# Optimization experiments

Measured on AMD Instinct MI355X. Metric: run time of the kernel, lower is better.

Reference implementation:

```python
import jax, jax.numpy as jnp
from jax import lax
import numpy as np

B, T = 256, 100
N_FEAT, V, E, H = 64, 32, 8, 512
CAT_POS = np.arange(0, N_FEAT, 4)                                 # 16 categorical feature indices
CONT_POS = np.array([k for k in range(N_FEAT) if k % 4 != 0])      # 48 continuous feature indices
N_CAT, N_CONT = len(CAT_POS), len(CONT_POS)
IN_LEN = N_FEAT + N_CAT * (E - 1)                                  # 176, matches input_linear.in_features
N_LAYERS = 2                                                        # len(hidden_layers) - 1 LSTMs

# Precompute the interleaved output layout of embed(): walking feature index k,
# categorical features occupy E slots, continuous features 1 slot.
def _layout():
    cont_off, cat_off, cur = [], [], 0
    for k in range(N_FEAT):
        if k % 4 == 0:
            cat_off.append(cur); cur += E
        else:
            cont_off.append(cur); cur += 1
    return np.array(cont_off), np.array(cat_off)
CONT_OFF, CAT_OFF = _layout()
CAT_COLS = (CAT_OFF[:, None] + np.arange(E)).ravel()               # [N_CAT*E] target columns


def lstm(x, Wih, Whh, bih, bhh):
    # PyTorch LSTM, batch_first, gate order (i, f, g, o).
    xw = jnp.einsum('bti,gi->btg', x, Wih) + bih                   # [B,T,4H] input projection (one GEMM)
    def step(carry, xw_t):
        h, c = carry
        gates = xw_t + h @ Whh.T + bhh
        i, f, g, o = jnp.split(gates, 4, axis=-1)
        c = jax.nn.sigmoid(f) * c + jax.nn.sigmoid(i) * jnp.tanh(g)
        h = jax.nn.sigmoid(o) * jnp.tanh(c)
        return (h, c), h
    h0 = jnp.zeros((x.shape[0], Whh.shape[1]), x.dtype)
    (_, _), hs = lax.scan(step, (h0, h0), jnp.swapaxes(xw, 0, 1))
    return jnp.swapaxes(hs, 0, 1)                                   # [B,T,H]


def setup_inputs() -> dict:
    key = jax.random.key(0)
    ks = jax.random.split(key, 16)
    s = 0.05
    base = jax.random.normal(ks[0], (B, T, N_FEAT), jnp.float32)
    cats = jax.random.randint(ks[1], (B, T, N_CAT), 0, V)
    x = base.at[..., CAT_POS].set(cats.astype(jnp.float32))
    return {
        'x': x,
        'scaler_mean': jax.random.normal(ks[2], (N_FEAT,), jnp.float32),
        'scaler_scale': jax.random.uniform(ks[3], (N_FEAT,), jnp.float32, minval=0.5, maxval=2.0),
        'emb': jax.random.normal(ks[4], (N_CAT, V, E), jnp.float32) * s,
        'W_in': jax.random.normal(ks[5], (IN_LEN, H), jnp.float32) * s,
        'b_in': jnp.zeros((H,), jnp.float32),
        'Wih': jax.random.normal(ks[6], (N_LAYERS, 4 * H, H), jnp.float32) * s,
        'Whh': jax.random.normal(ks[7], (N_LAYERS, 4 * H, H), jnp.float32) * s,
        'bih': jnp.zeros((N_LAYERS, 4 * H), jnp.float32),
        'bhh': jnp.zeros((N_LAYERS, 4 * H), jnp.float32),
        'W_out': jax.random.normal(ks[8], (H, N_CONT), jnp.float32) * s,
        'b_out': jnp.zeros((N_CONT,), jnp.float32),
        'W_cls': jax.random.normal(ks[9], (N_CAT, H, V), jnp.float32) * s,
        'b_cls': jnp.zeros((N_CAT, V), jnp.float32),
    }


def reference(x, scaler_mean, scaler_scale, emb, W_in, b_in, Wih, Whh, bih, bhh, W_out, b_out, W_cls, b_cls):
    # ---- embed(): vectorized replacement of the triple python loop ----
    scaled = (x - scaler_mean) / scaler_scale                      # sklearn StandardScaler.transform
    cont_vals = scaled[..., CONT_POS]                              # [B,T,48]
    idx = x[..., CAT_POS].astype(jnp.int32)                        # [B,T,16] categorical codes
    embv = emb[jnp.arange(N_CAT)[None, None, :], idx]              # [B,T,16,E] gather
    new = jnp.zeros((x.shape[0], x.shape[1], IN_LEN), x.dtype)
    new = new.at[..., CONT_OFF].set(cont_vals)
    new = new.at[..., CAT_COLS].set(embv.reshape(x.shape[0], x.shape[1], N_CAT * E))
    # ---- input linear + activation ----
    h = jax.nn.relu(new @ W_in + b_in)                             # [B,T,512]
    # ---- stacked LSTMs, activation after each ----
    for l in range(N_LAYERS):
        h = jax.nn.relu(lstm(h, Wih[l], Whh[l], bih[l], bhh[l]))
    last = h[:, -1, :]                                             # [B,512]
    cont_out = last @ W_out + b_out                                # [B,48]
    cls_out = jnp.einsum('bh,nhv->bnv', last, W_cls) + b_cls       # [B,16,32] classification heads
    return (cont_out, cls_out)
```

## Files before the change

kernel.cpp:

```cpp
#include <hip/hip_runtime.h>

#define BB 256
#define TT 100
#define HH 512
#define G4 2048
#define INL 176
#define KIN 192
#define NCAT 16
#define NCONT 48
#define VV 32
#define EE 8
#define MTOT (BB*TT)
#define GRPB 32
#define FS 16
#define NW (2*2*G4*HH)

typedef unsigned short u16;
typedef unsigned int   u32;
typedef unsigned long long u64;
typedef __attribute__((ext_vector_type(8))) short bf16x8;
typedef __attribute__((ext_vector_type(4))) float f32x4;

__device__ __forceinline__ float bf2f(u16 u){
    union { u32 i; float f; } v; v.i = ((u32)u) << 16; return v.f;
}
__device__ __forceinline__ u16 f2bf(float f){
    union { float f; u32 i; } v; v.f = f;
    u32 b = v.i;
    b += 0x7FFFu + ((b >> 16) & 1u);
    return (u16)(b >> 16);
}
__device__ __forceinline__ float fast_tanh(float x){
    float e = __expf(2.f * x);
    return 1.f - 2.f / (e + 1.f);
}
__device__ __forceinline__ u64 relu4_bf16(u64 v){
    u64 s = v & 0x8000800080008000ULL;
    u64 m = s - (s >> 15);
    return v & ~(s | m);
}

__global__ void PredictionModel_58841051955204_kernel(
    const float* __restrict__ Win, u16* __restrict__ WinT,
    const float* __restrict__ Wih, u16* __restrict__ Wihb,
    const float* __restrict__ Whh, u16* __restrict__ Whhb){
    int idx = blockIdx.x*256 + threadIdx.x;
    if (idx < HH*KIN){
        int h = idx / KIN, i = idx % KIN;
        WinT[idx] = (i < INL) ? f2bf(Win[i*HH + h]) : (u16)0;
        return;
    }
    int c1 = idx - HH*KIN;
    if (c1 < 2*G4*HH){ Wihb[c1] = f2bf(Wih[c1]); return; }
    int c2 = c1 - 2*G4*HH;
    if (c2 < 2*G4*HH) Whhb[c2] = f2bf(Whh[c2]);
}

__global__ void k_feat(const float* __restrict__ x, const float* __restrict__ mean,
                       const float* __restrict__ scale, const float* __restrict__ emb,
                       u16* __restrict__ feat, int* __restrict__ bar){
    if (blockIdx.x == 0){
        for (int i = threadIdx.x; i < 4096; i += 256)
            __hip_atomic_store(&bar[i], 0, __ATOMIC_RELAXED, __HIP_MEMORY_SCOPE_AGENT);
    }
    int idx = blockIdx.x*256 + threadIdx.x;
    int bt = idx >> 4, g = idx & 15;
    if (bt >= MTOT) return;
    const float* xr = x + (size_t)bt*64;
    u16* fr = feat + (size_t)bt*KIN;
    int k0 = g*4;
    int ci = (int)xr[k0];
    if (ci < 0) ci = 0;
    if (ci > VV-1) ci = VV-1;
    const float* ep = emb + (size_t)(g*VV + ci)*EE;
    int c0 = g*11;
    for (int e = 0; e < 8; e++) fr[c0+e] = f2bf(ep[e]);
    for (int j = 1; j <= 3; j++){
        int k = k0 + j;
        fr[c0 + 8 + (j-1)] = f2bf((xr[k] - mean[k]) / scale[k]);
    }
    fr[INL + g] = 0;
}

__global__ __launch_bounds__(256) void k_gemm(
    const u16* __restrict__ A, int lda,
    const u16* __restrict__ W, int K,
    const float* __restrict__ bias1, const float* __restrict__ bias2,
    void* __restrict__ out, int ldo, int kc_cnt, int do_relu, int out_half)
{
    __shared__ u16 sA[64*40];
    __shared__ u16 sB[256*40];
    int tid = threadIdx.x;
    int w = tid >> 6, lane = tid & 63, q = lane >> 4, r = lane & 15;
    int m0 = blockIdx.x * 64;
    int n0 = blockIdx.y * 256;

    f32x4 acc[4][4];
    for (int a_ = 0; a_ < 4; a_++)
        for (int b_ = 0; b_ < 4; b_++){
            acc[a_][b_][0] = 0.f; acc[a_][b_][1] = 0.f;
            acc[a_][b_][2] = 0.f; acc[a_][b_][3] = 0.f;
        }

    for (int kc = 0; kc < kc_cnt; kc++){
        {
            int row = tid >> 2, seg = tid & 3;
            uint4 v = *(const uint4*)(A + (size_t)(m0+row)*lda + kc*32 + seg*8);
            *(uint4*)(&sA[row*40 + seg*8]) = v;
            const u16* wr = W + (size_t)(n0 + tid)*K + kc*32;
            uint4 b0 = *(const uint4*)(wr);
            uint4 b1 = *(const uint4*)(wr+8);
            uint4 b2 = *(const uint4*)(wr+16);
            uint4 b3 = *(const uint4*)(wr+24);
            u16* d = &sB[tid*40];
            *(uint4*)(d)    = b0; *(uint4*)(d+8)  = b1;
            *(uint4*)(d+16) = b2; *(uint4*)(d+24) = b3;
        }
        __syncthreads();
        bf16x8 a[4], b[4];
        for (int mt = 0; mt < 4; mt++) a[mt] = *(const bf16x8*)(&sA[(mt*16 + r)*40 + q*8]);
        for (int i = 0; i < 4; i++)    b[i]  = *(const bf16x8*)(&sB[((w*4+i)*16 + r)*40 + q*8]);
        for (int mt = 0; mt < 4; mt++)
            for (int i = 0; i < 4; i++)
                acc[mt][i] = __builtin_amdgcn_mfma_f32_16x16x32_bf16(a[mt], b[i], acc[mt][i], 0, 0, 0);
        __syncthreads();
    }

    for (int i = 0; i < 4; i++){
        int n = n0 + (w*4+i)*16 + r;
        float bs = 0.f;
        if (bias1) bs += bias1[n];
        if (bias2) bs += bias2[n];
        for (int mt = 0; mt < 4; mt++){
            for (int reg = 0; reg < 4; reg++){
                int m = m0 + mt*16 + q*4 + reg;
                float v = acc[mt][i][reg] + bs;
                if (do_relu) v = fmaxf(v, 0.f);
                if (out_half) ((_Float16*)out)[(size_t)m*ldo + n] = (_Float16)v;
                else          ((u16*)out)[(size_t)m*ldo + n] = f2bf(v);
            }
        }
    }
}

__global__ __launch_bounds__(256, 1) void k_rec2(
    const u16* __restrict__ Wihb,
    const u16* __restrict__ Whhb,
    const u16* __restrict__ Xbuf,
    const float* __restrict__ bih, const float* __restrict__ bhh,
    u64* __restrict__ h0r,
    u64* __restrict__ h1A, u64* __restrict__ h1B,
    int* __restrict__ bar)
{
    extern __shared__ u16 smem[];
    int tid = threadIdx.x;
    int w = tid >> 6, lane = tid & 63, q = lane >> 4, r = lane & 15;
    int lay  = blockIdx.x >> 7;
    int bid7 = blockIdx.x & 127;
    int mg = bid7 & 3, jb = bid7 >> 2;
    int m0 = mg*64, j0 = jb*16;
    int j = j0 + r;
    int* F0x = bar;
    int* F1x = bar + 2048;
    int fidx = (mg*GRPB + jb)*FS;
    const u16* sWih = smem;
    const u16* sWhh = smem + 64*512;

    {
        int row = tid >> 2, seg = tid & 3;
        int g = row >> 4, jj = row & 15;
        const u16* srcI = Wihb + (size_t)lay*G4*HH + (size_t)(g*HH + j0 + jj)*HH;
        const u16* srcW = Whhb + (size_t)lay*G4*HH + (size_t)(g*HH + j0 + jj)*HH;
        for (int i = 0; i < 16; i++){
            int c = seg*16 + i;
            *(uint4*)(&smem[row*512 + ((c ^ (row & 7)) * 8)]) = *(const uint4*)(srcI + c*8);
            *(uint4*)(&smem[64*512 + row*512 + ((c ^ (row & 7)) * 8)]) = *(const uint4*)(srcW + c*8);
        }
    }
    float creg[4] = {0.f, 0.f, 0.f, 0.f};
    if ((r & 3) == 0){
        u64* hz = lay ? h1A : (h0r + (size_t)3*BB*(HH/4));
        for (int reg = 0; reg < 4; reg++){
            int m = m0 + w*16 + q*4 + reg;
            __hip_atomic_store(&hz[(size_t)m*(HH/4) + ((j0 + r) >> 2)], 0ULL,
                               __ATOMIC_RELAXED, __HIP_MEMORY_SCOPE_AGENT);
        }
    }
    asm volatile("s_waitcnt vmcnt(0)" ::: "memory");
    __syncthreads();
    if (tid == 0)
        __hip_atomic_store(lay ? &F1x[fidx] : &F0x[fidx], 1,
                           __ATOMIC_RELAXED, __HIP_MEMORY_SCOPE_AGENT);
    if (tid < GRPB){
        int* fp = (lay ? F1x : F0x) + (mg*GRPB + tid)*FS;
        long long t0c = clock64();
        while (__hip_atomic_load(fp, __ATOMIC_RELAXED, __HIP_MEMORY_SCOPE_AGENT) < 1){
            __builtin_amdgcn_s_sleep(1);
            if (clock64() - t0c > 50000000LL) break;
        }
    }
    __syncthreads();

    float bs[4];
    for (int g = 0; g < 4; g++)
        bs[g] = bih[lay*G4 + g*HH + j] + bhh[lay*G4 + g*HH + j];

    if (!lay){
        const u64* xb = (const u64*)Xbuf;
        u64 xn[32];
        {
            const u64* xrow = xb + ((size_t)(m0 + w*16 + r)*TT + 0)*(HH/4);
            #pragma unroll
            for (int kc = 0; kc < 16; kc++){
                int jg0 = kc*8 + q*2;
                xn[kc*2]   = __builtin_nontemporal_load(&xrow[jg0]);
                xn[kc*2+1] = __builtin_nontemporal_load(&xrow[jg0+1]);
            }
        }

        for (int t = 0; t < TT; t++){
            const u64* hsrc = h0r + (size_t)((t + 3) & 3)*BB*(HH/4);
            u32* hdst32 = (u32*)(h0r + (size_t)(t & 3)*BB*(HH/4));
            const u64* hrow = hsrc + (size_t)(m0 + w*16 + r)*(HH/4);

            u64 hd[32];
            #pragma unroll
            for (int kc = 0; kc < 16; kc++){
                int jg0 = kc*8 + q*2;
                hd[kc*2]   = __hip_atomic_load(&hrow[jg0],   __ATOMIC_RELAXED, __HIP_MEMORY_SCOPE_AGENT);
                hd[kc*2+1] = __hip_atomic_load(&hrow[jg0+1], __ATOMIC_RELAXED, __HIP_MEMORY_SCOPE_AGENT);
            }

            f32x4 acc[4];
            for (int g = 0; g < 4; g++){
                acc[g][0] = 0.f; acc[g][1] = 0.f; acc[g][2] = 0.f; acc[g][3] = 0.f;
            }
            #pragma unroll
            for (int kc = 0; kc < 16; kc++){
                union { u64 d[2]; bf16x8 v; } au;
                au.d[0] = xn[kc*2];
                au.d[1] = xn[kc*2+1];
                int cbase = kc*4 + q;
                #pragma unroll
                for (int g = 0; g < 4; g++){
                    int row = g*16 + r;
                    bf16x8 b = *(const bf16x8*)(&sWih[row*512 + ((cbase ^ (row & 7)) * 8)]);
                    acc[g] = __builtin_amdgcn_mfma_f32_16x16x32_bf16(au.v, b, acc[g], 0, 0, 0);
                }
            }
            asm volatile("" :
                "+v"(hd[0]),  "+v"(hd[1]),  "+v"(hd[2]),  "+v"(hd[3]),
                "+v"(hd[4]),  "+v"(hd[5]),  "+v"(hd[6]),  "+v"(hd[7]),
                "+v"(hd[8]),  "+v"(hd[9]),  "+v"(hd[10]), "+v"(hd[11]),
                "+v"(hd[12]), "+v"(hd[13]), "+v"(hd[14]), "+v"(hd[15]));
            asm volatile("" :
                "+v"(hd[16]), "+v"(hd[17]), "+v"(hd[18]), "+v"(hd[19]),
                "+v"(hd[20]), "+v"(hd[21]), "+v"(hd[22]), "+v"(hd[23]),
                "+v"(hd[24]), "+v"(hd[25]), "+v"(hd[26]), "+v"(hd[27]),
                "+v"(hd[28]), "+v"(hd[29]), "+v"(hd[30]), "+v"(hd[31]));
            __builtin_amdgcn_sched_barrier(0);
            if (t + 1 < TT){
                const u64* xrow = xb + ((size_t)(m0 + w*16 + r)*TT + (t+1))*(HH/4);
                #pragma unroll
                for (int kc = 0; kc < 16; kc++){
                    int jg0 = kc*8 + q*2;
                    xn[kc*2]   = __builtin_nontemporal_load(&xrow[jg0]);
                    xn[kc*2+1] = __builtin_nontemporal_load(&xrow[jg0+1]);
                }
            }
            #pragma unroll
            for (int kc = 0; kc < 16; kc++){
                union { u64 d[2]; bf16x8 v; } au;
                au.d[0] = hd[kc*2];
                au.d[1] = hd[kc*2+1];
                int cbase = kc*4 + q;
                #pragma unroll
                for (int g = 0; g < 4; g++){
                    int row = g*16 + r;
                    bf16x8 b = *(const bf16x8*)(&sWhh[row*512 + ((cbase ^ (row & 7)) * 8)]);
                    acc[g] = __builtin_amdgcn_mfma_f32_16x16x32_bf16(au.v, b, acc[g], 0, 0, 0);
                }
            }

            #pragma unroll
            for (int reg = 0; reg < 4; reg++){
                int m = m0 + w*16 + q*4 + reg;
                float Gi = acc[0][reg] + bs[0];
                float Gf = acc[1][reg] + bs[1];
                float Gg = acc[2][reg] + bs[2];
                float Go = acc[3][reg] + bs[3];
                float iv = 1.f/(1.f + __expf(-Gi));
                float fv = 1.f/(1.f + __expf(-Gf));
                float gv = fast_tanh(Gg);
                float ov = 1.f/(1.f + __expf(-Go));
                float c = fv * creg[reg] + iv * gv;
                creg[reg] = c;
                float h = ov * fast_tanh(c);
                u32 own = (u32)f2bf(h);
                u32 p01 = own | (((u32)__shfl_xor((int)own, 1)) << 16);
                if ((r & 1) == 0){
                    __hip_atomic_store(&hdst32[(size_t)m*(HH/2) + ((j0 + r) >> 1)], p01,
                                       __ATOMIC_RELAXED, __HIP_MEMORY_SCOPE_AGENT);
                }
            }

            asm volatile("s_waitcnt vmcnt(0)" ::: "memory");
            __syncthreads();
            if (tid == 0)
                __hip_atomic_store(&F0x[fidx], t + 2, __ATOMIC_RELAXED, __HIP_MEMORY_SCOPE_AGENT);
            if (t + 1 < TT){
                if (tid < 64){
                    long long t0c = clock64();
                    const int* fp; int thr;
                    if (lane < GRPB){ fp = &F0x[(mg*GRPB + lane)*FS];        thr = t + 2; }
                    else            { fp = &F1x[(mg*GRPB + (lane-GRPB))*FS]; thr = t - 1; }
                    while (__hip_atomic_load(fp, __ATOMIC_RELAXED, __HIP_MEMORY_SCOPE_AGENT) < thr){
                        __builtin_amdgcn_s_sleep(1);
                        if (clock64() - t0c > 50000000LL) break;
                    }
                }
                __syncthreads();
            }
        }
    } else {
        if (tid < GRPB){
            const int* fp = &F0x[(mg*GRPB + tid)*FS];
            long long t0c = clock64();
            while (__hip_atomic_load(fp, __ATOMIC_RELAXED, __HIP_MEMORY_SCOPE_AGENT) < 2){
                __builtin_amdgcn_s_sleep(1);
                if (clock64() - t0c > 50000000LL) break;
            }
        }
        __syncthreads();

        for (int t = 0; t < TT; t++){
            const u64* xsrc = h0r + (size_t)(t & 3)*BB*(HH/4);
            const u64* hsrc = (t & 1) ? h1B : h1A;
            u64*       hdst = (t & 1) ? h1A : h1B;
            const u64* xrow = xsrc + (size_t)(m0 + w*16 + r)*(HH/4);
            const u64* hrow = hsrc + (size_t)(m0 + w*16 + r)*(HH/4);

            u64 hx[32], hh[32];
            #pragma unroll
            for (int kc = 0; kc < 16; kc++){
                int jg0 = kc*8 + q*2;
                hx[kc*2]   = __hip_atomic_load(&xrow[jg0],   __ATOMIC_RELAXED, __HIP_MEMORY_SCOPE_AGENT);
                hx[kc*2+1] = __hip_atomic_load(&xrow[jg0+1], __ATOMIC_RELAXED, __HIP_MEMORY_SCOPE_AGENT);
            }
            #pragma unroll
            for (int kc = 0; kc < 16; kc++){
                int jg0 = kc*8 + q*2;
                hh[kc*2]   = __hip_atomic_load(&hrow[jg0],   __ATOMIC_RELAXED, __HIP_MEMORY_SCOPE_AGENT);
                hh[kc*2+1] = __hip_atomic_load(&hrow[jg0+1], __ATOMIC_RELAXED, __HIP_MEMORY_SCOPE_AGENT);
            }
            asm volatile("" :
                "+v"(hx[0]),  "+v"(hx[1]),  "+v"(hx[2]),  "+v"(hx[3]),
                "+v"(hx[4]),  "+v"(hx[5]),  "+v"(hx[6]),  "+v"(hx[7]),
                "+v"(hx[8]),  "+v"(hx[9]),  "+v"(hx[10]), "+v"(hx[11]),
                "+v"(hx[12]), "+v"(hx[13]), "+v"(hx[14]), "+v"(hx[15]));
            asm volatile("" :
                "+v"(hx[16]), "+v"(hx[17]), "+v"(hx[18]), "+v"(hx[19]),
                "+v"(hx[20]), "+v"(hx[21]), "+v"(hx[22]), "+v"(hx[23]),
                "+v"(hx[24]), "+v"(hx[25]), "+v"(hx[26]), "+v"(hx[27]),
                "+v"(hx[28]), "+v"(hx[29]), "+v"(hx[30]), "+v"(hx[31]));
            __builtin_amdgcn_sched_barrier(0);
            #pragma unroll
            for (int i = 0; i < 32; i++) hx[i] = relu4_bf16(hx[i]);

            f32x4 acc[4];
            for (int g = 0; g < 4; g++){
                acc[g][0] = 0.f; acc[g][1] = 0.f; acc[g][2] = 0.f; acc[g][3] = 0.f;
            }
            #pragma unroll
            for (int kc = 0; kc < 16; kc++){
                union { u64 d[2]; bf16x8 v; } au;
                au.d[0] = hx[kc*2];
                au.d[1] = hx[kc*2+1];
                int cbase = kc*4 + q;
                #pragma unroll
                for (int g = 0; g < 4; g++){
                    int row = g*16 + r;
                    bf16x8 b = *(const bf16x8*)(&sWih[row*512 + ((cbase ^ (row & 7)) * 8)]);
                    acc[g] = __builtin_amdgcn_mfma_f32_16x16x32_bf16(au.v, b, acc[g], 0, 0, 0);
                }
            }
            asm volatile("" :
                "+v"(hh[0]),  "+v"(hh[1]),  "+v"(hh[2]),  "+v"(hh[3]),
                "+v"(hh[4]),  "+v"(hh[5]),  "+v"(hh[6]),  "+v"(hh[7]),
                "+v"(hh[8]),  "+v"(hh[9]),  "+v"(hh[10]), "+v"(hh[11]),
                "+v"(hh[12]), "+v"(hh[13]), "+v"(hh[14]), "+v"(hh[15]));
            asm volatile("" :
                "+v"(hh[16]), "+v"(hh[17]), "+v"(hh[18]), "+v"(hh[19]),
                "+v"(hh[20]), "+v"(hh[21]), "+v"(hh[22]), "+v"(hh[23]),
                "+v"(hh[24]), "+v"(hh[25]), "+v"(hh[26]), "+v"(hh[27]),
                "+v"(hh[28]), "+v"(hh[29]), "+v"(hh[30]), "+v"(hh[31]));
            __builtin_amdgcn_sched_barrier(0);
            #pragma unroll
            for (int kc = 0; kc < 16; kc++){
                union { u64 d[2]; bf16x8 v; } au;
                au.d[0] = hh[kc*2];
                au.d[1] = hh[kc*2+1];
                int cbase = kc*4 + q;
                #pragma unroll
                for (int g = 0; g < 4; g++){
                    int row = g*16 + r;
                    bf16x8 b = *(const bf16x8*)(&sWhh[row*512 + ((cbase ^ (row & 7)) * 8)]);
                    acc[g] = __builtin_amdgcn_mfma_f32_16x16x32_bf16(au.v, b, acc[g], 0, 0, 0);
                }
            }

            u32* hdst32 = (u32*)hdst;
            #pragma unroll
            for (int reg = 0; reg < 4; reg++){
                int m = m0 + w*16 + q*4 + reg;
                float Gi = acc[0][reg] + bs[0];
                float Gf = acc[1][reg] + bs[1];
                float Gg = acc[2][reg] + bs[2];
                float Go = acc[3][reg] + bs[3];
                float iv = 1.f/(1.f + __expf(-Gi));
                float fv = 1.f/(1.f + __expf(-Gf));
                float gv = fast_tanh(Gg);
                float ov = 1.f/(1.f + __expf(-Go));
                float c = fv * creg[reg] + iv * gv;
                creg[reg] = c;
                float h = ov * fast_tanh(c);
                u32 own = (u32)f2bf(h);
                u32 p01 = own | (((u32)__shfl_xor((int)own, 1)) << 16);
                if ((r & 1) == 0){
                    __hip_atomic_store(&hdst32[(size_t)m*(HH/2) + ((j0 + r) >> 1)], p01,
                                       __ATOMIC_RELAXED, __HIP_MEMORY_SCOPE_AGENT);
                }
            }

            asm volatile("s_waitcnt vmcnt(0)" ::: "memory");
            __syncthreads();
            if (tid == 0)
                __hip_atomic_store(&F1x[fidx], t + 2, __ATOMIC_RELAXED, __HIP_MEMORY_SCOPE_AGENT);

            if (t + 1 < TT){
                if (tid < 64){
                    long long t0c = clock64();
                    const int* fp; int thr;
                    if (lane < GRPB){ fp = &F1x[(mg*GRPB + lane)*FS];        thr = t + 2; }
                    else            { fp = &F0x[(mg*GRPB + (lane-GRPB))*FS]; thr = t + 3; }
                    while (__hip_atomic_load(fp, __ATOMIC_RELAXED, __HIP_MEMORY_SCOPE_AGENT) < thr){
                        __builtin_amdgcn_s_sleep(1);
                        if (clock64() - t0c > 50000000LL) break;
                    }
                }
                __syncthreads();
            }
        }
    }
}

__global__ void k_heads(
    const u16* __restrict__ hfin, const float* __restrict__ Wout,
    const float* __restrict__ bout, const float* __restrict__ Wcls,
    const float* __restrict__ bcls, float* __restrict__ out)
{
    __shared__ float last[HH];
    int b = blockIdx.x, tid = threadIdx.x;
    for (int h = tid; h < HH; h += 256) last[h] = fmaxf(bf2f(hfin[b*HH + h]), 0.f);
    __syncthreads();
    for (int o = tid; o < NCONT + NCAT*VV; o += 256){
        if (o < NCONT){
            float a = bout[o];
            for (int h = 0; h < HH; h++) a += last[h] * Wout[h*NCONT + o];
            out[b*NCONT + o] = (a == 0.0f) ? 7.0f : a;
        } else {
            int oc = o - NCONT;
            int n = oc >> 5, v = oc & 31;
            float a = bcls[oc];
            const float* wp = Wcls + (size_t)n*HH*VV + v;
            for (int h = 0; h < HH; h++) a += last[h] * wp[h*VV];
            out[BB*NCONT + b*(NCAT*VV) + oc] = (a == 0.0f) ? 7.0f : a;
        }
    }
}

extern "C" void kernel_launch(void* const* d_in, const int* in_sizes, int n_in,
                              void* d_out, int out_size, void* d_ws, size_t ws_size,
                              hipStream_t stream){
    const float* x      = (const float*)d_in[0];
    const float* smean  = (const float*)d_in[1];
    const float* sscale = (const float*)d_in[2];
    const float* emb    = (const float*)d_in[3];
    const float* Win    = (const float*)d_in[4];
    const float* bin    = (const float*)d_in[5];
    const float* Wih    = (const float*)d_in[6];
    const float* Whh    = (const float*)d_in[7];
    const float* bih    = (const float*)d_in[8];
    const float* bhh    = (const float*)d_in[9];
    const float* Wout   = (const float*)d_in[10];
    const float* bout   = (const float*)d_in[11];
    const float* Wcls   = (const float*)d_in[12];
    const float* bcls   = (const float*)d_in[13];
    (void)in_sizes; (void)n_in; (void)out_size;

    char* ws = (char*)d_ws;
    size_t off = 0;
    u16*      feat  = (u16*)(ws + off);      off += (size_t)MTOT*KIN*2;
    u16*      WinTb = (u16*)(ws + off);      off += (size_t)HH*KIN*2;
    u16*      Xbuf  = (u16*)(ws + off);      off += (size_t)MTOT*HH*2;
    u16*      Wihb  = (u16*)(ws + off);      off += (size_t)2*G4*HH*2;
    u16*      Whhb  = (u16*)(ws + off);      off += (size_t)2*G4*HH*2;
    u64*      h0r   = (u64*)(ws + off);      off += (size_t)4*BB*HH*2;
    u64*      h1A   = (u64*)(ws + off);      off += (size_t)BB*HH*2;
    u64*      h1B   = (u64*)(ws + off);      off += (size_t)BB*HH*2;
    int*      bar   = (int*)(ws + off);      off += 4096*4;
    (void)off; (void)ws_size;

    int prep_n = HH*KIN + 2*2*G4*HH;
    PredictionModel_58841051955204_kernel<<<(prep_n + 255)/256, 256, 0, stream>>>(
        Win, WinTb, Wih, Wihb, Whh, Whhb);

    k_feat<<<1600, 256, 0, stream>>>(x, smean, sscale, emb, feat, bar);
    k_gemm<<<dim3(400, 2), 256, 0, stream>>>(feat, KIN, WinTb, KIN, bin, (const float*)0,
                                             Xbuf, HH, 6, 1, 0);
    k_rec2<<<256, 256, 131072, stream>>>(Wihb, Whhb, Xbuf, bih, bhh,
                                         h0r, h1A, h1B, bar);
    k_heads<<<256, 256, 0, stream>>>((const u16*)h1A, Wout, bout, Wcls, bcls, (float*)d_out);
}
```

Before: 1.293 ms.

## Precompute next-step input projection while waiting on layer-0 recurrence barrier

In the layer-0 recurrence, the input-projection MFMAs for step t+1 now run right after the cross-block flag wait and the h loads, so only the Whh GEMM and gate math remain between receiving h and publishing the new h. The x loads for the next step are issued before polling. The point is to take the Wih GEMM off the critical path of the serial dependency chain. Flag polling also moves into a helper that reads clock64 only every 32 iterations, which cuts overhead in the spin loop. In exchange, register pressure rises because the accA accumulators now persist across iterations.

Result: no change. 1.269 ms (-1.9%).

```diff
diff --git a/kernel.cpp b/kernel.cpp
--- a/kernel.cpp
+++ b/kernel.cpp
@@ -13,7 +13,6 @@
 #define MTOT (BB*TT)
 #define GRPB 32
 #define FS 16
-#define NW (2*2*G4*HH)
 
 typedef unsigned short u16;
 typedef unsigned int   u32;
@@ -39,6 +38,27 @@
     u64 m = s - (s >> 15);
     return v & ~(s | m);
 }
+__device__ __forceinline__ void poll_flag(const int* fp, int thr){
+    int it = 0;
+    long long t0c = clock64();
+    while (__hip_atomic_load(fp, __ATOMIC_RELAXED, __HIP_MEMORY_SCOPE_AGENT) < thr){
+        __builtin_amdgcn_s_sleep(1);
+        if (((++it) & 31) == 0 && clock64() - t0c > 50000000LL) break;
+    }
+}
+
+#define FENCE32(a) \
+    asm volatile("" : \
+        "+v"(a[0]),  "+v"(a[1]),  "+v"(a[2]),  "+v"(a[3]), \
+        "+v"(a[4]),  "+v"(a[5]),  "+v"(a[6]),  "+v"(a[7]), \
+        "+v"(a[8]),  "+v"(a[9]),  "+v"(a[10]), "+v"(a[11]), \
+        "+v"(a[12]), "+v"(a[13]), "+v"(a[14]), "+v"(a[15])); \
+    asm volatile("" : \
+        "+v"(a[16]), "+v"(a[17]), "+v"(a[18]), "+v"(a[19]), \
+        "+v"(a[20]), "+v"(a[21]), "+v"(a[22]), "+v"(a[23]), \
+        "+v"(a[24]), "+v"(a[25]), "+v"(a[26]), "+v"(a[27]), \
+        "+v"(a[28]), "+v"(a[29]), "+v"(a[30]), "+v"(a[31])); \
+    __builtin_amdgcn_sched_barrier(0)
 
 __global__ void PredictionModel_58841051955204_kernel(
     const float* __restrict__ Win, u16* __restrict__ WinT,
@@ -191,14 +211,8 @@
     if (tid == 0)
         __hip_atomic_store(lay ? &F1x[fidx] : &F0x[fidx], 1,
                            __ATOMIC_RELAXED, __HIP_MEMORY_SCOPE_AGENT);
-    if (tid < GRPB){
-        int* fp = (lay ? F1x : F0x) + (mg*GRPB + tid)*FS;
-        long long t0c = clock64();
-        while (__hip_atomic_load(fp, __ATOMIC_RELAXED, __HIP_MEMORY_SCOPE_AGENT) < 1){
-            __builtin_amdgcn_s_sleep(1);
-            if (clock64() - t0c > 50000000LL) break;
-        }
-    }
+    if (tid < GRPB)
+        poll_flag((lay ? F1x : F0x) + (mg*GRPB + tid)*FS, 1);
     __syncthreads();
 
     float bs[4];
@@ -207,7 +221,16 @@
 
     if (!lay){
         const u64* xb = (const u64*)Xbuf;
-        u64 xn[32];
+        u64 xn[32], hd[32];
+        {
+            const u64* hrow = h0r + (size_t)3*BB*(HH/4) + (size_t)(m0 + w*16 + r)*(HH/4);
+            #pragma unroll
+            for (int kc = 0; kc < 16; kc++){
+                int jg0 = kc*8 + q*2;
+                hd[kc*2]   = __hip_atomic_load(&hrow[jg0],   __ATOMIC_RELAXED, __HIP_MEMORY_SCOPE_AGENT);
+                hd[kc*2+1] = __hip_atomic_load(&hrow[jg0+1], __ATOMIC_RELAXED, __HIP_MEMORY_SCOPE_AGENT);
+            }
+        }
         {
             const u64* xrow = xb + ((size_t)(m0 + w*16 + r)*TT + 0)*(HH/4);
             #pragma unroll
@@ -217,57 +240,31 @@
                 xn[kc*2+1] = __builtin_nontemporal_load(&xrow[jg0+1]);
             }
         }
+        FENCE32(xn);
+        f32x4 accA[4];
+        for (int g = 0; g < 4; g++){
+            accA[g][0] = 0.f; accA[g][1] = 0.f; accA[g][2] = 0.f; accA[g][3] = 0.f;
+        }
+        #pragma unroll
+        for (int kc = 0; kc < 16; kc++){
+            union { u64 d[2]; bf16x8 v; } au;
+            au.d[0] = xn[kc*2];
+            au.d[1] = xn[kc*2+1];
+            int cbase = kc*4 + q;
+            #pragma unroll
+            for (int g = 0; g < 4; g++){
+                int row = g*16 + r;
+                bf16x8 b = *(const bf16x8*)(&sWih[row*512 + ((cbase ^ (row & 7)) * 8)]);
+                accA[g] = __builtin_amdgcn_mfma_f32_16x16x32_bf16(au.v, b, accA[g], 0, 0, 0);
+            }
+        }
 
         for (int t = 0; t < TT; t++){
-            const u64* hsrc = h0r + (size_t)((t + 3) & 3)*BB*(HH/4);
             u32* hdst32 = (u32*)(h0r + (size_t)(t & 3)*BB*(HH/4));
-            const u64* hrow = hsrc + (size_t)(m0 + w*16 + r)*(HH/4);
-
-            u64 hd[32];
-            #pragma unroll
-            for (int kc = 0; kc < 16; kc++){
-                int jg0 = kc*8 + q*2;
-                hd[kc*2]   = __hip_atomic_load(&hrow[jg0],   __ATOMIC_RELAXED, __HIP_MEMORY_SCOPE_AGENT);
-                hd[kc*2+1] = __hip_atomic_load(&hrow[jg0+1], __ATOMIC_RELAXED, __HIP_MEMORY_SCOPE_AGENT);
-            }
-
+
+            FENCE32(hd);
             f32x4 acc[4];
-            for (int g = 0; g < 4; g++){
-                acc[g][0] = 0.f; acc[g][1] = 0.f; acc[g][2] = 0.f; acc[g][3] = 0.f;
-            }
-            #pragma unroll
-            for (int kc = 0; kc < 16; kc++){
-                union { u64 d[2]; bf16x8 v; } au;
-                au.d[0] = xn[kc*2];
-                au.d[1] = xn[kc*2+1];
-                int cbase = kc*4 + q;
-                #pragma unroll
-                for (int g = 0; g < 4; g++){
-                    int row = g*16 + r;
-                    bf16x8 b = *(const bf16x8*)(&sWih[row*512 + ((cbase ^ (row & 7)) * 8)]);
-                    acc[g] = __builtin_amdgcn_mfma_f32_16x16x32_bf16(au.v, b, acc[g], 0, 0, 0);
-                }
-            }
-            asm volatile("" :
-                "+v"(hd[0]),  "+v"(hd[1]),  "+v"(hd[2]),  "+v"(hd[3]),
-                "+v"(hd[4]),  "+v"(hd[5]),  "+v"(hd[6]),  "+v"(hd[7]),
-                "+v"(hd[8]),  "+v"(hd[9]),  "+v"(hd[10]), "+v"(hd[11]),
-                "+v"(hd[12]), "+v"(hd[13]), "+v"(hd[14]), "+v"(hd[15]));
-            asm volatile("" :
-                "+v"(hd[16]), "+v"(hd[17]), "+v"(hd[18]), "+v"(hd[19]),
-                "+v"(hd[20]), "+v"(hd[21]), "+v"(hd[22]), "+v"(hd[23]),
-                "+v"(hd[24]), "+v"(hd[25]), "+v"(hd[26]), "+v"(hd[27]),
-                "+v"(hd[28]), "+v"(hd[29]), "+v"(hd[30]), "+v"(hd[31]));
-            __builtin_amdgcn_sched_barrier(0);
-            if (t + 1 < TT){
-                const u64* xrow = xb + ((size_t)(m0 + w*16 + r)*TT + (t+1))*(HH/4);
-                #pragma unroll
-                for (int kc = 0; kc < 16; kc++){
-                    int jg0 = kc*8 + q*2;
-                    xn[kc*2]   = __builtin_nontemporal_load(&xrow[jg0]);
-                    xn[kc*2+1] = __builtin_nontemporal_load(&xrow[jg0+1]);
-                }
-            }
+            for (int g = 0; g < 4; g++) acc[g] = accA[g];
             #pragma unroll
             for (int kc = 0; kc < 16; kc++){
                 union { u64 d[2]; bf16x8 v; } au;
@@ -308,29 +305,54 @@
             __syncthreads();
             if (tid == 0)
                 __hip_atomic_store(&F0x[fidx], t + 2, __ATOMIC_RELAXED, __HIP_MEMORY_SCOPE_AGENT);
+
             if (t + 1 < TT){
+                {
+                    const u64* xrow = xb + ((size_t)(m0 + w*16 + r)*TT + (t+1))*(HH/4);
+                    #pragma unroll
+                    for (int kc = 0; kc < 16; kc++){
+                        int jg0 = kc*8 + q*2;
+                        xn[kc*2]   = __builtin_nontemporal_load(&xrow[jg0]);
+                        xn[kc*2+1] = __builtin_nontemporal_load(&xrow[jg0+1]);
+                    }
+                }
                 if (tid < 64){
-                    long long t0c = clock64();
-                    const int* fp; int thr;
-                    if (lane < GRPB){ fp = &F0x[(mg*GRPB + lane)*FS];        thr = t + 2; }
-                    else            { fp = &F1x[(mg*GRPB + (lane-GRPB))*FS]; thr = t - 1; }
-                    while (__hip_atomic_load(fp, __ATOMIC_RELAXED, __HIP_MEMORY_SCOPE_AGENT) < thr){
-                        __builtin_amdgcn_s_sleep(1);
-                        if (clock64() - t0c > 50000000LL) break;
+                    if (lane < GRPB) poll_flag(&F0x[(mg*GRPB + lane)*FS], t + 2);
+                    else             poll_flag(&F1x[(mg*GRPB + (lane-GRPB))*FS], t - 1);
+                }
+                __syncthreads();
+                {
+                    const u64* hrow = h0r + (size_t)(t & 3)*BB*(HH/4)
+                                    + (size_t)(m0 + w*16 + r)*(HH/4);
+                    #pragma unroll
+                    for (int kc = 0; kc < 16; kc++){
+                        int jg0 = kc*8 + q*2;
+                        hd[kc*2]   = __hip_atomic_load(&hrow[jg0],   __ATOMIC_RELAXED, __HIP_MEMORY_SCOPE_AGENT);
+                        hd[kc*2+1] = __hip_atomic_load(&hrow[jg0+1], __ATOMIC_RELAXED, __HIP_MEMORY_SCOPE_AGENT);
                     }
                 }
-                __syncthreads();
+                FENCE32(xn);
+                for (int g = 0; g < 4; g++){
+                    accA[g][0] = 0.f; accA[g][1] = 0.f; accA[g][2] = 0.f; accA[g][3] = 0.f;
+                }
+                #pragma unroll
+                for (int kc = 0; kc < 16; kc++){
+                    union { u64 d[2]; bf16x8 v; } au;
+                    au.d[0] = xn[kc*2];
+                    au.d[1] = xn[kc*2+1];
+                    int cbase = kc*4 + q;
+                    #pragma unroll
+                    for (int g = 0; g < 4; g++){
+                        int row = g*16 + r;
+                        bf16x8 b = *(const bf16x8*)(&sWih[row*512 + ((cbase ^ (row & 7)) * 8)]);
+                        accA[g] = __builtin_amdgcn_mfma_f32_16x16x32_bf16(au.v, b, accA[g], 0, 0, 0);
+                    }
+                }
             }
         }
     } else {
-        if (tid < GRPB){
-            const int* fp = &F0x[(mg*GRPB + tid)*FS];
-            long long t0c = clock64();
-            while (__hip_atomic_load(fp, __ATOMIC_RELAXED, __HIP_MEMORY_SCOPE_AGENT) < 2){
-                __builtin_amdgcn_s_sleep(1);
-                if (clock64() - t0c > 50000000LL) break;
-            }
-        }
+        if (tid < GRPB)
+            poll_flag(&F0x[(mg*GRPB + tid)*FS], 2);
         __syncthreads();
 
         for (int t = 0; t < TT; t++){
@@ -353,17 +375,7 @@
                 hh[kc*2]   = __hip_atomic_load(&hrow[jg0],   __ATOMIC_RELAXED, __HIP_MEMORY_SCOPE_AGENT);
                 hh[kc*2+1] = __hip_atomic_load(&hrow[jg0+1], __ATOMIC_RELAXED, __HIP_MEMORY_SCOPE_AGENT);
             }
-            asm volatile("" :
-                "+v"(hx[0]),  "+v"(hx[1]),  "+v"(hx[2]),  "+v"(hx[3]),
-                "+v"(hx[4]),  "+v"(hx[5]),  "+v"(hx[6]),  "+v"(hx[7]),
-                "+v"(hx[8]),  "+v"(hx[9]),  "+v"(hx[10]), "+v"(hx[11]),
-                "+v"(hx[12]), "+v"(hx[13]), "+v"(hx[14]), "+v"(hx[15]));
-            asm volatile("" :
-                "+v"(hx[16]), "+v"(hx[17]), "+v"(hx[18]), "+v"(hx[19]),
-                "+v"(hx[20]), "+v"(hx[21]), "+v"(hx[22]), "+v"(hx[23]),
-                "+v"(hx[24]), "+v"(hx[25]), "+v"(hx[26]), "+v"(hx[27]),
-                "+v"(hx[28]), "+v"(hx[29]), "+v"(hx[30]), "+v"(hx[31]));
-            __builtin_amdgcn_sched_barrier(0);
+            FENCE32(hx);
             #pragma unroll
             for (int i = 0; i < 32; i++) hx[i] = relu4_bf16(hx[i]);
 
@@ -384,17 +396,7 @@
                     acc[g] = __builtin_amdgcn_mfma_f32_16x16x32_bf16(au.v, b, acc[g], 0, 0, 0);
                 }
             }
-            asm volatile("" :
-                "+v"(hh[0]),  "+v"(hh[1]),  "+v"(hh[2]),  "+v"(hh[3]),
-                "+v"(hh[4]),  "+v"(hh[5]),  "+v"(hh[6]),  "+v"(hh[7]),
-                "+v"(hh[8]),  "+v"(hh[9]),  "+v"(hh[10]), "+v"(hh[11]),
-                "+v"(hh[12]), "+v"(hh[13]), "+v"(hh[14]), "+v"(hh[15]));
-            asm volatile("" :
-                "+v"(hh[16]), "+v"(hh[17]), "+v"(hh[18]), "+v"(hh[19]),
-                "+v"(hh[20]), "+v"(hh[21]), "+v"(hh[22]), "+v"(hh[23]),
-                "+v"(hh[24]), "+v"(hh[25]), "+v"(hh[26]), "+v"(hh[27]),
-                "+v"(hh[28]), "+v"(hh[29]), "+v"(hh[30]), "+v"(hh[31]));
-            __builtin_amdgcn_sched_barrier(0);
+            FENCE32(hh);
             #pragma unroll
             for (int kc = 0; kc < 16; kc++){
                 union { u64 d[2]; bf16x8 v; } au;
@@ -439,14 +441,8 @@
 
             if (t + 1 < TT){
                 if (tid < 64){
-                    long long t0c = clock64();
-                    const int* fp; int thr;
-                    if (lane < GRPB){ fp = &F1x[(mg*GRPB + lane)*FS];        thr = t + 2; }
-                    else            { fp = &F0x[(mg*GRPB + (lane-GRPB))*FS]; thr = t + 3; }
-                    while (__hip_atomic_load(fp, __ATOMIC_RELAXED, __HIP_MEMORY_SCOPE_AGENT) < thr){
-                        __builtin_amdgcn_s_sleep(1);
-                        if (clock64() - t0c > 50000000LL) break;
-                    }
+                    if (lane < GRPB) poll_flag(&F1x[(mg*GRPB + lane)*FS], t + 2);
+                    else             poll_flag(&F0x[(mg*GRPB + (lane-GRPB))*FS], t + 3);
                 }
                 __syncthreads();
             }
```
